# Kernel tuning notes

Measured on AMD Instinct MI355X. Metric: run time of the kernel, lower is better.

## Reference

```python
import jax, jax.numpy as jnp
import numpy as np

EPS = 1e-6
H, KV, HD = 16, 4, 64      # q heads, kv heads, head dim
BLK = 32                   # dllm_block_length (block-diffusion attention)
TOPK = 2                   # experts per token

def rmsnorm(x, w):
    return x * jax.lax.rsqrt(jnp.mean(x * x, axis=-1, keepdims=True) + EPS) * w

def rotate_half(x):
    x1, x2 = jnp.split(x, 2, axis=-1)
    return jnp.concatenate([-x2, x1], axis=-1)

def setup_inputs() -> dict:
    key = jax.random.key(0)
    ks = jax.random.split(key, 12)
    B, S, D = 1, 2048, 1024
    E, I = 8, 1024
    s = 0.02
    pos = jnp.arange(S, dtype=jnp.float32)
    inv_freq = 1.0 / (10000.0 ** (jnp.arange(0, HD, 2, dtype=jnp.float32) / HD))
    emb = jnp.concatenate([jnp.outer(pos, inv_freq)] * 2, axis=-1)  # [S, HD]
    return {
        'hidden_states': jax.random.normal(ks[0], (B, S, D), jnp.float32),
        'cos': jnp.cos(emb), 'sin': jnp.sin(emb),
        'w_qkv': jax.random.normal(ks[1], (D, (H + 2 * KV) * HD), jnp.float32) * s,
        'w_o': jax.random.normal(ks[2], (H * HD, D), jnp.float32) * s,
        'q_norm_w': jnp.ones((HD,), jnp.float32),
        'k_norm_w': jnp.ones((HD,), jnp.float32),
        'in_ln_w': jnp.ones((D,), jnp.float32),
        'post_ln_w': jnp.ones((D,), jnp.float32),
        'router_w': jax.random.normal(ks[3], (D, E), jnp.float32) * s,
        'w_gate': jax.random.normal(ks[4], (E, D, I), jnp.float32) * s,
        'w_up': jax.random.normal(ks[5], (E, D, I), jnp.float32) * s,
        'w_down': jax.random.normal(ks[6], (E, I, D), jnp.float32) * s,
        'ws_gate': jax.random.normal(ks[7], (D, I), jnp.float32) * s,
        'ws_up': jax.random.normal(ks[8], (D, I), jnp.float32) * s,
        'ws_down': jax.random.normal(ks[9], (I, D), jnp.float32) * s,
    }

def reference(hidden_states, cos, sin, w_qkv, w_o, q_norm_w, k_norm_w, in_ln_w,
              post_ln_w, router_w, w_gate, w_up, w_down, ws_gate, ws_up, ws_down):
    B, S, D = hidden_states.shape
    scale = HD ** -0.5
    # --- attention (pre-norm) ---
    h = rmsnorm(hidden_states, in_ln_w)
    qkv = h @ w_qkv
    q, k, v = jnp.split(qkv, [H * HD, (H + KV) * HD], axis=-1)
    q = q.reshape(B, S, H, HD); k = k.reshape(B, S, KV, HD); v = v.reshape(B, S, KV, HD)
    q = rmsnorm(q, q_norm_w); k = rmsnorm(k, k_norm_w)   # qk-norm per head
    c = cos[None, :, None, :]; sn = sin[None, :, None, :]
    q = q * c + rotate_half(q) * sn
    k = k * c + rotate_half(k) * sn
    rep = H // KV
    k = jnp.repeat(k, rep, axis=2); v = jnp.repeat(v, rep, axis=2)  # GQA expand
    scores = jnp.einsum('bqhd,bkhd->bhqk', q, k) * scale
    blk = jnp.arange(S) // BLK
    mask = blk[:, None] >= blk[None, :]   # block-causal: full attn inside block
    scores = jnp.where(mask[None, None], scores, jnp.float32(-1e30))
    p = jax.nn.softmax(scores, axis=-1)
    attn = jnp.einsum('bhqk,bkhd->bqhd', p, v).reshape(B, S, H * HD)
    x = hidden_states + attn @ w_o
    # --- MoE FFN (pre-norm) ---
    h2 = rmsnorm(x, post_ln_w)
    t = h2.reshape(B * S, D)
    logits = t.astype(jnp.float32) @ router_w.astype(jnp.float32)  # fp32 router
    probs = jax.nn.softmax(logits, axis=-1)
    topv, topi = jax.lax.top_k(probs, TOPK)
    topv = topv / jnp.sum(topv, axis=-1, keepdims=True)            # norm_topk_prob
    E = router_w.shape[1]
    w_tok = jnp.zeros((t.shape[0], E), jnp.float32).at[
        jnp.arange(t.shape[0])[:, None], topi].set(topv).astype(t.dtype)
    g = jnp.einsum('td,edi->tei', t, w_gate)
    u = jnp.einsum('td,edi->tei', t, w_up)
    eo = jnp.einsum('tei,eid->ted', jax.nn.silu(g) * u, w_down)
    moe = jnp.einsum('te,ted->td', w_tok, eo)
    shared = (jax.nn.silu(t @ ws_gate) * (t @ ws_up)) @ ws_down
    return x + (moe + shared).reshape(B, S, D)
```

## Files before the change

### kernel.cpp

```cpp
#include <hip/hip_runtime.h>
#include <hip/hip_bf16.h>
#include <math.h>

#define S 2048
#define D 1024
#define NH 16
#define NKV 4
#define HD 64
#define QKV_N 1536
#define NE 8
#define NI 1024
#define EPS 1e-6f

typedef __bf16 bf16_t;
typedef __bf16 __attribute__((may_alias)) abf16;
typedef __attribute__((ext_vector_type(8))) __bf16 bf16x8;
typedef __attribute__((ext_vector_type(4))) float f32x4;
union I4B8 { int4 i; bf16x8 v; bf16_t e[8]; };

__device__ __forceinline__ void gll16(const void* g, void* l) {
  __builtin_amdgcn_global_load_lds(
      (const __attribute__((address_space(1))) void*)g,
      (__attribute__((address_space(3))) void*)l, 16, 0, 0);
}


__global__ void rmsnorm_router_kernel(const float* __restrict__ in, const float* __restrict__ w,
                                      const float* __restrict__ rw,
                                      __hip_bfloat16* __restrict__ out16,
                                      int* __restrict__ topk_e, float* __restrict__ topk_w) {
  int t = blockIdx.x;
  int tid = threadIdx.x;
  const float* row = in + (size_t)t * D;
  float v[4];
  float ss = 0.f;
#pragma unroll
  for (int i = 0; i < 4; ++i) {
    v[i] = row[tid + i * 256];
    ss += v[i] * v[i];
  }
#pragma unroll
  for (int off = 32; off; off >>= 1) ss += __shfl_xor(ss, off);
  __shared__ float wsum[4];
  __shared__ float pl[4][NE];
  int wave = tid >> 6, lane = tid & 63;
  if (lane == 0) wsum[wave] = ss;
  __syncthreads();
  float tot = wsum[0] + wsum[1] + wsum[2] + wsum[3];
  float r = rsqrtf(tot / (float)D + EPS);
  float p[NE] = {};
#pragma unroll
  for (int i = 0; i < 4; ++i) {
    int d = tid + i * 256;
    float val = v[i] * r * w[d];
    out16[(size_t)t * D + d] = __float2bfloat16(val);
    const float* rwd = rw + (size_t)d * NE;
#pragma unroll
    for (int e = 0; e < NE; ++e) p[e] += val * rwd[e];
  }
#pragma unroll
  for (int off = 32; off; off >>= 1)
#pragma unroll
    for (int e = 0; e < NE; ++e) p[e] += __shfl_xor(p[e], off);
  if (lane == 0)
#pragma unroll
    for (int e = 0; e < NE; ++e) pl[wave][e] = p[e];
  __syncthreads();
  if (tid == 0) {
    float q[NE];
#pragma unroll
    for (int e = 0; e < NE; ++e) q[e] = pl[0][e] + pl[1][e] + pl[2][e] + pl[3][e];
    float mx = q[0];
#pragma unroll
    for (int e = 1; e < NE; ++e) mx = fmaxf(mx, q[e]);
    float ex[NE];
#pragma unroll
    for (int e = 0; e < NE; ++e) ex[e] = __expf(q[e] - mx);
    int e0 = 0;
#pragma unroll
    for (int e = 1; e < NE; ++e) if (ex[e] > ex[e0]) e0 = e;
    int e1 = (e0 == 0) ? 1 : 0;
#pragma unroll
    for (int e = 0; e < NE; ++e) if (e != e0 && ex[e] > ex[e1]) e1 = e;
    float w0 = ex[e0] / (ex[e0] + ex[e1]);
    float w1 = ex[e1] / (ex[e0] + ex[e1]);
    topk_e[2 * t] = e0;  topk_e[2 * t + 1] = e1;
    topk_w[2 * t] = w0;  topk_w[2 * t + 1] = w1;
  }
}

__global__ void transpose_all_kernel(
    const float* __restrict__ w_qkv, const float* __restrict__ w_o,
    const float* __restrict__ w_gate, const float* __restrict__ w_up,
    const float* __restrict__ w_down, const float* __restrict__ ws_gate,
    const float* __restrict__ ws_up, const float* __restrict__ ws_down,
    __hip_bfloat16* wqkvT, __hip_bfloat16* woT, __hip_bfloat16* wgT,
    __hip_bfloat16* wuT, __hip_bfloat16* wdT, __hip_bfloat16* wsgT,
    __hip_bfloat16* wsuT, __hip_bfloat16* wsdT,
    const float* __restrict__ hidden, const float* __restrict__ in_ln,
    __hip_bfloat16* __restrict__ hb_out) {
  int z = blockIdx.z;
  int tid = threadIdx.x;
  if (z == 29) {
    __shared__ float wsum[4];
    int base = ((int)blockIdx.y * 24 + (int)blockIdx.x) * 6;
    int wave = tid >> 6;
#pragma unroll
    for (int jj = 0; jj < 6; ++jj) {
      int t = base + jj;
      if (t < S) {
        const float* row = hidden + (size_t)t * D;
        float v[4];
        float ss = 0.f;
#pragma unroll
        for (int i = 0; i < 4; ++i) {
          v[i] = row[tid + i * 256];
          ss += v[i] * v[i];
        }
#pragma unroll
        for (int off = 32; off; off >>= 1) ss += __shfl_xor(ss, off);
        if ((tid & 63) == 0) wsum[wave] = ss;
        __syncthreads();
        float tot = wsum[0] + wsum[1] + wsum[2] + wsum[3];
        float r = rsqrtf(tot / (float)D + EPS);
#pragma unroll
        for (int i = 0; i < 4; ++i) {
          int d = tid + i * 256;
          hb_out[(size_t)t * D + d] = __float2bfloat16(v[i] * r * in_ln[d]);
        }
      }
      __syncthreads();
    }
    return;
  }
  __shared__ bf16_t tileb[64 * 66];
  const float* W; __hip_bfloat16* WT; int Kd, Nd;
  if (z == 0)       { W = w_qkv;  WT = wqkvT; Kd = D;  Nd = QKV_N; }
  else if (z == 1)  { W = w_o;    WT = woT;   Kd = D;  Nd = D; }
  else if (z < 10)  { int e = z - 2;  W = w_gate + (size_t)e * D * NI; WT = wgT + (size_t)e * D * NI; Kd = D;  Nd = NI; }
  else if (z < 18)  { int e = z - 10; W = w_up   + (size_t)e * D * NI; WT = wuT + (size_t)e * D * NI; Kd = D;  Nd = NI; }
  else if (z < 26)  { int e = z - 18; W = w_down + (size_t)e * NI * D; WT = wdT + (size_t)e * NI * D; Kd = NI; Nd = D; }
  else if (z == 26) { W = ws_gate; WT = wsgT; Kd = D;  Nd = NI; }
  else if (z == 27) { W = ws_up;   WT = wsuT; Kd = D;  Nd = NI; }
  else              { W = ws_down; WT = wsdT; Kd = NI; Nd = D; }
  int n0 = blockIdx.x * 64, k0 = blockIdx.y * 64;
  if (n0 >= Nd || k0 >= Kd) return;
  int nq = tid & 15;
  int kq = tid >> 4;
  bf16_t b[4][4];
#pragma unroll
  for (int i = 0; i < 4; ++i) {
    float4 v = *(const float4*)(W + (size_t)(k0 + kq * 4 + i) * Nd + n0 + nq * 4);
    b[i][0] = (bf16_t)v.x; b[i][1] = (bf16_t)v.y;
    b[i][2] = (bf16_t)v.z; b[i][3] = (bf16_t)v.w;
  }
#pragma unroll
  for (int j = 0; j < 4; ++j) {
    union { bf16_t e[2]; int q; } p0, p1;
    p0.e[0] = b[0][j]; p0.e[1] = b[1][j];
    p1.e[0] = b[2][j]; p1.e[1] = b[3][j];
    int nrow = nq * 4 + j;
    *(int*)&tileb[nrow * 66 + kq * 4]     = p0.q;
    *(int*)&tileb[nrow * 66 + kq * 4 + 2] = p1.q;
  }
  __syncthreads();
  int n = tid >> 2;
  int kc = (tid & 3) * 16;
  union { bf16_t e[16]; int4 q[2]; } pk;
#pragma unroll
  for (int r = 0; r < 8; ++r)
    *(int*)&pk.e[r * 2] = *(const int*)&tileb[n * 66 + kc + r * 2];
  int4* outp = (int4*)(WT + (size_t)(n0 + n) * Kd + k0 + kc);
  outp[0] = pk.q[0];
  outp[1] = pk.q[1];
}

__global__ __launch_bounds__(256) void mgemm_kernel(
    const __hip_bfloat16* __restrict__ A, const __hip_bfloat16* __restrict__ BT,
    const float* __restrict__ Cadd, float* __restrict__ C,
    int M, int N, int K,
    const int* __restrict__ counts, const int* __restrict__ offsets,
    const int* __restrict__ tok, int a_comp,
    const __hip_bfloat16* __restrict__ As2, const __hip_bfloat16* __restrict__ BTs2,
    float* __restrict__ Cs2) {
  __shared__ __align__(16) bf16_t Asd[2][128 * 32];
  __shared__ __align__(16) bf16_t Bsd[2][128 * 32];
  __shared__ int rowmap[128];
  int e = blockIdx.z;
  bool sh = (counts != nullptr) && (e == NE);
  int cnt = sh ? M : (counts ? counts[e] : M);
  int bm = blockIdx.y * 128;
  if (bm >= cnt) return;
  int bn = blockIdx.x * 128;
  int obase = sh ? 0 : (offsets ? offsets[e] : 0);
  const bf16_t* Ab = sh ? (const bf16_t*)As2 : (const bf16_t*)A;
  const bf16_t* BTe = sh ? (const bf16_t*)BTs2 : ((const bf16_t*)BT + (size_t)e * N * K);
  float* Cp = sh ? Cs2 : C;
  const int* toke = (!sh && tok) ? tok + e * S : nullptr;
  int acompe = sh ? 0 : a_comp;
  int tid = threadIdx.x;
  if (tid < 128) {
    int gp = bm + tid;
    int cp = gp < cnt ? gp : cnt - 1;
    rowmap[tid] = toke ? toke[cp] : (acompe ? obase + cp : cp);
  }
  __syncthreads();
  int wave = tid >> 6, lane = tid & 63;
  int quad = lane >> 4, l16 = lane & 15;
  int wm = wave >> 1, wn = wave & 1;
  int srow = tid >> 2, scol = (tid & 3) * 8;
  size_t aoff0 = (size_t)rowmap[srow] * K + scol;
  size_t aoff1 = (size_t)rowmap[64 + srow] * K + scol;
  size_t boff0 = (size_t)(bn + srow) * K + scol;
  size_t boff1 = (size_t)(bn + 64 + srow) * K + scol;
  f32x4 acc[4][4];
#pragma unroll
  for (int i = 0; i < 4; ++i)
#pragma unroll
    for (int j = 0; j < 4; ++j) acc[i][j] = (f32x4){0.f, 0.f, 0.f, 0.f};

  {
    char* AsB = (char*)Asd[0] + wave * 1024;
    char* BsB = (char*)Bsd[0] + wave * 1024;
    gll16(Ab + aoff0, AsB);
    gll16(Ab + aoff1, AsB + 4096);
    gll16(BTe + boff0, BsB);
    gll16(BTe + boff1, BsB + 4096);
  }
  for (int k0 = 0; k0 < K; k0 += 32) {
    int cur = (k0 >> 5) & 1;
    __syncthreads();
    if (k0 + 32 < K) {
      char* AsB = (char*)Asd[cur ^ 1] + wave * 1024;
      char* BsB = (char*)Bsd[cur ^ 1] + wave * 1024;
      gll16(Ab + aoff0 + k0 + 32, AsB);
      gll16(Ab + aoff1 + k0 + 32, AsB + 4096);
      gll16(BTe + boff0 + k0 + 32, BsB);
      gll16(BTe + boff1 + k0 + 32, BsB + 4096);
    }
    I4B8 af[4], bfr[4];
#pragma unroll
    for (int i = 0; i < 4; ++i)
      af[i].i = *(const int4*)(Asd[cur] + (wm * 64 + i * 16 + l16) * 32 + quad * 8);
#pragma unroll
    for (int j = 0; j < 4; ++j)
      bfr[j].i = *(const int4*)(Bsd[cur] + (wn * 64 + j * 16 + l16) * 32 + quad * 8);
#pragma unroll
    for (int i = 0; i < 4; ++i)
#pragma unroll
      for (int j = 0; j < 4; ++j)
        acc[i][j] = __builtin_amdgcn_mfma_f32_16x16x32_bf16(af[i].v, bfr[j].v, acc[i][j], 0, 0, 0);
  }
#pragma unroll
  for (int i = 0; i < 4; ++i) {
#pragma unroll
    for (int r = 0; r < 4; ++r) {
      int trow = wm * 64 + i * 16 + quad * 4 + r;
      int gp = bm + trow;
      if (gp < cnt) {
        size_t rowb = (size_t)(obase + gp) * N;
#pragma unroll
        for (int j = 0; j < 4; ++j) {
          int col = bn + wn * 64 + j * 16 + l16;
          size_t idx = rowb + col;
          Cp[idx] = acc[i][j][r] + (Cadd ? Cadd[idx] : 0.f);
        }
      }
    }
  }
}

__global__ __launch_bounds__(256) void mgemm_n64_kernel(
    const __hip_bfloat16* __restrict__ A, const __hip_bfloat16* __restrict__ BT,
    const float* __restrict__ Cadd, float* __restrict__ C,
    int M, int N, int K) {
  __shared__ __align__(16) bf16_t Asd[2][128 * 32];
  __shared__ __align__(16) bf16_t Bsd[2][64 * 32];
  int bm = blockIdx.y * 128;
  int bn = blockIdx.x * 64;
  int tid = threadIdx.x;
  int wave = tid >> 6, lane = tid & 63;
  int quad = lane >> 4, l16 = lane & 15;
  int wm = wave >> 1, wn = wave & 1;
  int srow = tid >> 2, scol = (tid & 3) * 8;
  size_t aoff0 = (size_t)(bm + srow) * K + scol;
  size_t aoff1 = (size_t)(bm + 64 + srow) * K + scol;
  size_t boff = (size_t)(bn + srow) * K + scol;
  const bf16_t* Ab = (const bf16_t*)A;
  const bf16_t* Bb = (const bf16_t*)BT;
  f32x4 acc[4][2];
#pragma unroll
  for (int i = 0; i < 4; ++i)
#pragma unroll
    for (int j = 0; j < 2; ++j) acc[i][j] = (f32x4){0.f, 0.f, 0.f, 0.f};
  {
    char* AsB = (char*)Asd[0] + wave * 1024;
    gll16(Ab + aoff0, AsB);
    gll16(Ab + aoff1, AsB + 4096);
    gll16(Bb + boff, (char*)Bsd[0] + wave * 1024);
  }
  for (int k0 = 0; k0 < K; k0 += 32) {
    int cur = (k0 >> 5) & 1;
    __syncthreads();
    if (k0 + 32 < K) {
      char* AsB = (char*)Asd[cur ^ 1] + wave * 1024;
      gll16(Ab + aoff0 + k0 + 32, AsB);
      gll16(Ab + aoff1 + k0 + 32, AsB + 4096);
      gll16(Bb + boff + k0 + 32, (char*)Bsd[cur ^ 1] + wave * 1024);
    }
    I4B8 af[4], bf[2];
#pragma unroll
    for (int i = 0; i < 4; ++i)
      af[i].i = *(const int4*)(Asd[cur] + (wm * 64 + i * 16 + l16) * 32 + quad * 8);
#pragma unroll
    for (int j = 0; j < 2; ++j)
      bf[j].i = *(const int4*)(Bsd[cur] + (wn * 32 + j * 16 + l16) * 32 + quad * 8);
#pragma unroll
    for (int i = 0; i < 4; ++i)
#pragma unroll
      for (int j = 0; j < 2; ++j)
        acc[i][j] = __builtin_amdgcn_mfma_f32_16x16x32_bf16(af[i].v, bf[j].v, acc[i][j], 0, 0, 0);
  }
#pragma unroll
  for (int i = 0; i < 4; ++i) {
#pragma unroll
    for (int r = 0; r < 4; ++r) {
      int gp = bm + wm * 64 + i * 16 + quad * 4 + r;
      size_t rowb = (size_t)gp * N;
#pragma unroll
      for (int j = 0; j < 2; ++j) {
        int col = bn + wn * 32 + j * 16 + l16;
        size_t idx = rowb + col;
        C[idx] = acc[i][j][r] + (Cadd ? Cadd[idx] : 0.f);
      }
    }
  }
}

__global__ __launch_bounds__(256) void mgemm_gu_kernel(
    const __hip_bfloat16* __restrict__ A, const __hip_bfloat16* __restrict__ BTg,
    const __hip_bfloat16* __restrict__ BTu, __hip_bfloat16* __restrict__ act,
    int M, int N, int K,
    const int* __restrict__ counts, const int* __restrict__ offsets,
    const int* __restrict__ tok,
    const __hip_bfloat16* __restrict__ BTgs, const __hip_bfloat16* __restrict__ BTus,
    __hip_bfloat16* __restrict__ acts) {
  __shared__ __align__(16) bf16_t Asd[2][128 * 32];
  __shared__ __align__(16) bf16_t Bgd[2][64 * 32];
  __shared__ __align__(16) bf16_t Bud[2][64 * 32];
  __shared__ int rowmap[128];
  int e = blockIdx.z;
  bool sh = (counts != nullptr) && (e == NE);
  int cnt = sh ? M : (counts ? counts[e] : M);
  int bm = blockIdx.y * 128;
  if (bm >= cnt) return;
  int bn = blockIdx.x * 64;
  const bf16_t* Ab = (const bf16_t*)A;
  const bf16_t* Bg = sh ? (const bf16_t*)BTgs : ((const bf16_t*)BTg + (size_t)e * N * K);
  const bf16_t* Bu = sh ? (const bf16_t*)BTus : ((const bf16_t*)BTu + (size_t)e * N * K);
  bf16_t* outp = sh ? (bf16_t*)acts : (bf16_t*)act;
  int obase = sh ? 0 : (offsets ? offsets[e] : 0);
  const int* toke = (!sh && tok) ? tok + e * S : nullptr;
  int tid = threadIdx.x;
  if (tid < 128) {
    int gp = bm + tid;
    int cp = gp < cnt ? gp : cnt - 1;
    rowmap[tid] = toke ? toke[cp] : cp;
  }
  __syncthreads();
  int wave = tid >> 6, lane = tid & 63;
  int quad = lane >> 4, l16 = lane & 15;
  int wm = wave >> 1, wn = wave & 1;
  int srow = tid >> 2, scol = (tid & 3) * 8;
  size_t aoff0 = (size_t)rowmap[srow] * K + scol;
  size_t aoff1 = (size_t)rowmap[64 + srow] * K + scol;
  size_t boff = (size_t)(bn + srow) * K + scol;
  f32x4 accg[4][2], accu[4][2];
#pragma unroll
  for (int i = 0; i < 4; ++i)
#pragma unroll
    for (int j = 0; j < 2; ++j) {
      accg[i][j] = (f32x4){0.f, 0.f, 0.f, 0.f};
      accu[i][j] = (f32x4){0.f, 0.f, 0.f, 0.f};
    }
  {
    char* AsB = (char*)Asd[0] + wave * 1024;
    gll16(Ab + aoff0, AsB);
    gll16(Ab + aoff1, AsB + 4096);
    gll16(Bg + boff, (char*)Bgd[0] + wave * 1024);
    gll16(Bu + boff, (char*)Bud[0] + wave * 1024);
  }
  for (int k0 = 0; k0 < K; k0 += 32) {
    int cur = (k0 >> 5) & 1;
    __syncthreads();
    if (k0 + 32 < K) {
      char* AsB = (char*)Asd[cur ^ 1] + wave * 1024;
      gll16(Ab + aoff0 + k0 + 32, AsB);
      gll16(Ab + aoff1 + k0 + 32, AsB + 4096);
      gll16(Bg + boff + k0 + 32, (char*)Bgd[cur ^ 1] + wave * 1024);
      gll16(Bu + boff + k0 + 32, (char*)Bud[cur ^ 1] + wave * 1024);
    }
    I4B8 af[4], bg[2], bu[2];
#pragma unroll
    for (int i = 0; i < 4; ++i)
      af[i].i = *(const int4*)(Asd[cur] + (wm * 64 + i * 16 + l16) * 32 + quad * 8);
#pragma unroll
    for (int j = 0; j < 2; ++j) {
      bg[j].i = *(const int4*)(Bgd[cur] + (wn * 32 + j * 16 + l16) * 32 + quad * 8);
      bu[j].i = *(const int4*)(Bud[cur] + (wn * 32 + j * 16 + l16) * 32 + quad * 8);
    }
#pragma unroll
    for (int i = 0; i < 4; ++i)
#pragma unroll
      for (int j = 0; j < 2; ++j) {
        accg[i][j] = __builtin_amdgcn_mfma_f32_16x16x32_bf16(af[i].v, bg[j].v, accg[i][j], 0, 0, 0);
        accu[i][j] = __builtin_amdgcn_mfma_f32_16x16x32_bf16(af[i].v, bu[j].v, accu[i][j], 0, 0, 0);
      }
  }
#pragma unroll
  for (int i = 0; i < 4; ++i) {
#pragma unroll
    for (int r = 0; r < 4; ++r) {
      int trow = wm * 64 + i * 16 + quad * 4 + r;
      int gp = bm + trow;
      if (gp < cnt) {
        size_t rowb = (size_t)(obase + gp) * N;
#pragma unroll
        for (int j = 0; j < 2; ++j) {
          int col = bn + wn * 32 + j * 16 + l16;
          float g = accg[i][j][r], uu = accu[i][j][r];
          float sg = g / (1.f + __expf(-g));
          outp[rowb + col] = __float2bfloat16(sg * uu);
        }
      }
    }
  }
}

__global__ void qkv_post_kernel(const float* __restrict__ qkv,
                                const float* __restrict__ qw, const float* __restrict__ kw,
                                const float* __restrict__ cosb, const float* __restrict__ sinb,
                                __hip_bfloat16* __restrict__ qout,
                                __hip_bfloat16* __restrict__ kout,
                                __hip_bfloat16* __restrict__ vT) {
  __shared__ float tile[32][33];
  if (blockIdx.y == 5) {
    int bx = blockIdx.x;
    if (bx < 512) {
      int t0 = (bx & 63) * 32;
      int c0 = (bx >> 6) * 32;
      int tx = threadIdx.x & 31, ty = threadIdx.x >> 5;
#pragma unroll
      for (int i = 0; i < 4; ++i)
        tile[ty + i * 8][tx] = qkv[(size_t)(t0 + ty + i * 8) * QKV_N + (NH + NKV) * HD + c0 + tx];
      __syncthreads();
#pragma unroll
      for (int i = 0; i < 4; ++i)
        vT[(size_t)(c0 + ty + i * 8) * S + t0 + tx] = __float2bfloat16(tile[tx][ty + i * 8]);
    }
    return;
  }
  int t = blockIdx.x;
  int u = blockIdx.y * 4 + (threadIdx.x >> 6);
  int lane = threadIdx.x & 63;
  bool isq = (u < NH);
  int h = isq ? u : (u - NH);
  size_t src = (size_t)t * QKV_N + (isq ? (h * HD) : (NH * HD + h * HD)) + lane;
  float xv = qkv[src];
  float ss = xv * xv;
#pragma unroll
  for (int off = 32; off; off >>= 1) ss += __shfl_xor(ss, off);
  float r = rsqrtf(ss * (1.f / 64.f) + EPS);
  float xn = xv * r * (isq ? qw[lane] : kw[lane]);
  float other = __shfl_xor(xn, 32);
  float rot = (lane < 32) ? -other : other;
  float res = xn * cosb[t * 64 + lane] + rot * sinb[t * 64 + lane];
  if (isq) qout[(size_t)t * (NH * HD) + h * HD + lane] = __float2bfloat16(res * 0.125f);
  else     kout[(size_t)t * (NKV * HD) + h * HD + lane] = __float2bfloat16(res);
}

__global__ __launch_bounds__(256) void attn_kernel(
    const __hip_bfloat16* __restrict__ qg, const __hip_bfloat16* __restrict__ kg,
    const __hip_bfloat16* __restrict__ vT,
    float* __restrict__ op0, float* __restrict__ op1,
    float* __restrict__ op2, float* __restrict__ op3,
    float* __restrict__ mpart, float* __restrict__ lpart) {
  int qt = (int)(gridDim.x - 1) - (int)blockIdx.x;
  int kvh = blockIdx.y;
  int z = blockIdx.z;
  int tid = threadIdx.x;
  int wave = tid >> 6, lane = tid & 63;
  int quad = lane >> 4, l16 = lane & 15;
  int h = kvh * 4 + wave;

  float* opz = (z == 0) ? op0 : (z == 1) ? op1 : (z == 2) ? op2 : op3;
  float* mp = mpart + (size_t)z * S * NH;
  float* lp = lpart + (size_t)z * S * NH;

  int nb = (qt >> 1) + 1;
  int nt = (nb + 1) >> 1;
  bool halfm = (nb & 1) != 0;
  int lo = (nt * z) >> 2;
  int hi = (nt * (z + 1)) >> 2;

  if (lo >= hi) {
    int row = qt * 16 + (tid >> 4);
    float* od = opz + (size_t)row * (NH * HD) + kvh * 256 + (tid & 15) * 16;
    int4 zz = {0, 0, 0, 0};
#pragma unroll
    for (int i = 0; i < 4; ++i) *(int4*)(od + i * 4) = zz;
    if (tid < 64) {
      int rr = qt * 16 + (tid >> 2), hh = kvh * 4 + (tid & 3);
      mp[(size_t)rr * NH + hh] = -1e30f;
      lp[(size_t)rr * NH + hh] = 0.f;
    }
    return;
  }

  __shared__ __align__(16) int KsI[64 * 36];
  __shared__ __align__(16) int VTI[64 * 36];
  __shared__ __align__(16) int PsI[4][16 * 36];

  I4B8 qf[2];
#pragma unroll
  for (int ch = 0; ch < 2; ++ch)
    qf[ch].i = *(const int4*)((const abf16*)qg +
        (size_t)(qt * 16 + l16) * (NH * HD) + h * HD + ch * 32 + quad * 8);

  I4B8 ones;
  ones.i = (int4){0x3F803F80, 0x3F803F80, 0x3F803F80, 0x3F803F80};

  float m_r[4];
  f32x4 o[4], o4;
#pragma unroll
  for (int r = 0; r < 4; ++r) m_r[r] = -1e30f;
#pragma unroll
  for (int sub = 0; sub < 4; ++sub) o[sub] = (f32x4){0.f, 0.f, 0.f, 0.f};
  o4 = (f32x4){0.f, 0.f, 0.f, 0.f};

  int sp = tid >> 3, sc = tid & 7;
  const abf16* kb = (const abf16*)kg;
  const abf16* vb = (const abf16*)vT;

  int4 rk0 = *(const int4*)(kb + (size_t)(lo * 64 + sp) * (NKV * HD) + kvh * HD + sc * 8);
  int4 rk1 = *(const int4*)(kb + (size_t)(lo * 64 + 32 + sp) * (NKV * HD) + kvh * HD + sc * 8);
  int4 rv0 = *(const int4*)(vb + (size_t)(kvh * HD + sp) * S + lo * 64 + sc * 8);
  int4 rv1 = *(const int4*)(vb + (size_t)(kvh * HD + 32 + sp) * S + lo * 64 + sc * 8);

  for (int kc = lo; kc < hi; ++kc) {
    *(int4*)&KsI[sp * 36 + sc * 4] = rk0;
    *(int4*)&KsI[(sp + 32) * 36 + sc * 4] = rk1;
    *(int4*)&VTI[sp * 36 + sc * 4] = rv0;
    *(int4*)&VTI[(sp + 32) * 36 + sc * 4] = rv1;
    __syncthreads();

    if (kc + 1 < hi) {
      rk0 = *(const int4*)(kb + (size_t)((kc + 1) * 64 + sp) * (NKV * HD) + kvh * HD + sc * 8);
      rk1 = *(const int4*)(kb + (size_t)((kc + 1) * 64 + 32 + sp) * (NKV * HD) + kvh * HD + sc * 8);
      rv0 = *(const int4*)(vb + (size_t)(kvh * HD + sp) * S + (kc + 1) * 64 + sc * 8);
      rv1 = *(const int4*)(vb + (size_t)(kvh * HD + 32 + sp) * S + (kc + 1) * 64 + sc * 8);
    }

    f32x4 s[4];
#pragma unroll
    for (int sub = 0; sub < 4; ++sub) s[sub] = (f32x4){0.f, 0.f, 0.f, 0.f};
    __builtin_amdgcn_s_setprio(1);
#pragma unroll
    for (int sub = 0; sub < 4; ++sub)
#pragma unroll
      for (int ch = 0; ch < 2; ++ch) {
        I4B8 ku;
        ku.i = *(const int4*)&KsI[(sub * 16 + l16) * 36 + ch * 16 + quad * 4];
        s[sub] = __builtin_amdgcn_mfma_f32_16x16x32_bf16(qf[ch].v, ku.v, s[sub], 0, 0, 0);
      }
    __builtin_amdgcn_s_setprio(0);
    if (halfm && kc == nt - 1) {
#pragma unroll
      for (int r = 0; r < 4; ++r) { s[2][r] = -1e30f; s[3][r] = -1e30f; }
    }

    abf16* pw = (abf16*)PsI[wave];
#pragma unroll
    for (int r = 0; r < 4; ++r) {
      float v = fmaxf(fmaxf(s[0][r], s[1][r]), fmaxf(s[2][r], s[3][r]));
#pragma unroll
      for (int off = 1; off < 16; off <<= 1) v = fmaxf(v, __shfl_xor(v, off));
      float mx = fmaxf(m_r[r], v);
      float al = __expf(m_r[r] - mx);
      m_r[r] = mx;
      float p0 = __expf(s[0][r] - mx);
      float p1 = __expf(s[1][r] - mx);
      float p2 = __expf(s[2][r] - mx);
      float p3 = __expf(s[3][r] - mx);
      int prow = quad * 4 + r;
      pw[prow * 72 + l16]      = (bf16_t)p0;
      pw[prow * 72 + 16 + l16] = (bf16_t)p1;
      pw[prow * 72 + 32 + l16] = (bf16_t)p2;
      pw[prow * 72 + 48 + l16] = (bf16_t)p3;
      o4[r] *= al;
#pragma unroll
      for (int sub = 0; sub < 4; ++sub) o[sub][r] *= al;
    }

    I4B8 pu[2];
#pragma unroll
    for (int ch = 0; ch < 2; ++ch)
      pu[ch].i = *(const int4*)&PsI[wave][l16 * 36 + ch * 16 + quad * 4];
    __builtin_amdgcn_s_setprio(1);
#pragma unroll
    for (int sub = 0; sub < 4; ++sub)
#pragma unroll
      for (int ch = 0; ch < 2; ++ch) {
        I4B8 vf;
        vf.i = *(const int4*)&VTI[(sub * 16 + l16) * 36 + ch * 16 + quad * 4];
        o[sub] = __builtin_amdgcn_mfma_f32_16x16x32_bf16(pu[ch].v, vf.v, o[sub], 0, 0, 0);
      }
#pragma unroll
    for (int ch = 0; ch < 2; ++ch)
      o4 = __builtin_amdgcn_mfma_f32_16x16x32_bf16(pu[ch].v, ones.v, o4, 0, 0, 0);
    __builtin_amdgcn_s_setprio(0);
    __syncthreads();
  }

#pragma unroll
  for (int r = 0; r < 4; ++r) {
    int row = qt * 16 + quad * 4 + r;
    float* od = opz + (size_t)row * (NH * HD) + h * HD;
#pragma unroll
    for (int sub = 0; sub < 4; ++sub)
      od[sub * 16 + l16] = o[sub][r];
    if (l16 == 0) {
      mp[(size_t)row * NH + h] = m_r[r];
      lp[(size_t)row * NH + h] = o4[r];
    }
  }
}

__global__ void attn_merge_kernel(const float* __restrict__ op0,
                                  const float* __restrict__ op1,
                                  const float* __restrict__ op2,
                                  const float* __restrict__ op3,
                                  const float* __restrict__ mpart,
                                  const float* __restrict__ lpart,
                                  __hip_bfloat16* __restrict__ attn) {
  int row = blockIdx.x;
  int tid = threadIdx.x;
#pragma unroll
  for (int i = 0; i < 4; ++i) {
    int c = tid + i * 256;
    int h = c >> 6;
    float m0 = mpart[(size_t)row * NH + h];
    float m1 = mpart[(size_t)(S + row) * NH + h];
    float m2 = mpart[(size_t)(2 * S + row) * NH + h];
    float m3 = mpart[(size_t)(3 * S + row) * NH + h];
    float l0 = lpart[(size_t)row * NH + h];
    float l1 = lpart[(size_t)(S + row) * NH + h];
    float l2 = lpart[(size_t)(2 * S + row) * NH + h];
    float l3 = lpart[(size_t)(3 * S + row) * NH + h];
    float M = fmaxf(fmaxf(m0, m1), fmaxf(m2, m3));
    float a0 = __expf(m0 - M), a1 = __expf(m1 - M);
    float a2 = __expf(m2 - M), a3 = __expf(m3 - M);
    float l = l0 * a0 + l1 * a1 + l2 * a2 + l3 * a3;
    size_t idx = (size_t)row * (NH * HD) + c;
    float v = (op0[idx] * a0 + op1[idx] * a1 + op2[idx] * a2 + op3[idx] * a3) / l;
    attn[idx] = __float2bfloat16(v);
  }
}

__global__ __launch_bounds__(1024) void router_place_kernel(
    const int* __restrict__ topk_e, int* __restrict__ counts, int* __restrict__ offsets,
    int* __restrict__ tok_list, int* __restrict__ topk_pos) {
  __shared__ int lcnt[NE];
  int tid = threadIdx.x;
  int lane = tid & 63;
  if (tid < NE) lcnt[tid] = 0;
  __syncthreads();
#pragma unroll
  for (int r = 0; r < 2; ++r) {
    int t = r * 1024 + tid;
#pragma unroll
    for (int s = 0; s < 2; ++s) {
      int e = topk_e[2 * t + s];
      int pos = 0;
#pragma unroll
      for (int x = 0; x < NE; ++x) {
        unsigned long long mask = __ballot(e == x);
        if (mask) {
          int leader = __ffsll((unsigned long long)mask) - 1;
          int cnt = __popcll(mask);
          int base = 0;
          if (lane == leader) base = atomicAdd(&lcnt[x], cnt);
          base = __shfl(base, leader);
          if (e == x)
            pos = base + __popcll(mask & ((1ull << lane) - 1ull));
        }
      }
      topk_pos[2 * t + s] = pos;
      tok_list[e * S + pos] = t;
    }
  }
  __syncthreads();
  if (tid == 0) {
    int acc = 0;
    for (int e = 0; e < NE; ++e) { offsets[e] = acc; counts[e] = lcnt[e]; acc += lcnt[e]; }
  }
}

__global__ void final_kernel(const float* __restrict__ x, const float* __restrict__ sout,
                             const float* __restrict__ eo,
                             const int* __restrict__ topk_e, const int* __restrict__ topk_pos,
                             const float* __restrict__ topk_w, const int* __restrict__ offsets,
                             float* __restrict__ out) {
  int t = blockIdx.x;
  int tid = threadIdx.x;
  int e0 = topk_e[2 * t], e1 = topk_e[2 * t + 1];
  size_t r0 = (size_t)offsets[e0] + topk_pos[2 * t];
  size_t r1 = (size_t)offsets[e1] + topk_pos[2 * t + 1];
  float w0 = topk_w[2 * t], w1 = topk_w[2 * t + 1];
#pragma unroll
  for (int i = 0; i < 4; ++i) {
    int d = tid + i * 256;
    size_t idx = (size_t)t * D + d;
    out[idx] = x[idx] + sout[idx] + w0 * eo[r0 * D + d] + w1 * eo[r1 * D + d];
  }
}

extern "C" void kernel_launch(void* const* d_in, const int* in_sizes, int n_in,
                              void* d_out, int out_size, void* d_ws, size_t ws_size,
                              hipStream_t stream) {
  const float* hidden  = (const float*)d_in[0];
  const float* cosb    = (const float*)d_in[1];
  const float* sinb    = (const float*)d_in[2];
  const float* w_qkv   = (const float*)d_in[3];
  const float* w_o     = (const float*)d_in[4];
  const float* q_norm  = (const float*)d_in[5];
  const float* k_norm  = (const float*)d_in[6];
  const float* in_ln   = (const float*)d_in[7];
  const float* post_ln = (const float*)d_in[8];
  const float* router_w= (const float*)d_in[9];
  const float* w_gate  = (const float*)d_in[10];
  const float* w_up    = (const float*)d_in[11];
  const float* w_down  = (const float*)d_in[12];
  const float* ws_gate = (const float*)d_in[13];
  const float* ws_up   = (const float*)d_in[14];
  const float* ws_down = (const float*)d_in[15];
  float* out = (float*)d_out;
  float* ws = (float*)d_ws;

  typedef __hip_bfloat16 hbf;
  hbf* wqkvT = (hbf*)(ws);
  hbf* woT   = (hbf*)(ws +  768 * 1024);
  hbf* wgT   = (hbf*)(ws + 1280 * 1024);
  hbf* wuT   = (hbf*)(ws + 5376 * 1024);
  hbf* wdT   = (hbf*)(ws + 9472 * 1024);
  hbf* wsgT  = (hbf*)(ws + 13568 * 1024);
  hbf* wsuT  = (hbf*)(ws + 14080 * 1024);
  hbf* wsdT  = (hbf*)(ws + 14592 * 1024);
  hbf*   hb      = (hbf*)(ws + 15104 * 1024);
  float* qkv     = ws + 16128 * 1024;
  hbf*   qbB     = (hbf*)(ws + 19200 * 1024);
  hbf*   kbB     = (hbf*)(ws + 20224 * 1024);
  hbf*   vTb     = (hbf*)(ws + 20480 * 1024);
  hbf*   attnb16 = (hbf*)(ws + 20736 * 1024);
  float* x       = ws + 22784 * 1024;
  hbf*   h2b     = (hbf*)(ws + 26880 * 1024);
  hbf*   act     = (hbf*)(ws + 16128 * 1024);
  float* eo      = ws + 18176 * 1024;
  hbf*   sact    = (hbf*)(ws + 27904 * 1024);
  float* sout    = ws + 28928 * 1024;
  float* mpart   = ws + 15104 * 1024;
  float* lpart   = mpart + 4 * S * NH;
  float* opart0  = ws + 16128 * 1024;
  float* opart1  = ws + 22784 * 1024;
  float* opart2  = ws + 28928 * 1024;
  float* opart3  = ws + 26880 * 1024;
  int* counts   = (int*)(ws + 30976 * 1024);
  int* offsets  = counts + NE;
  int* tok_list = offsets + NE;
  int* topk_e   = tok_list + NE * S;
  int* topk_pos = topk_e + 2 * S;
  float* topk_w = (float*)(topk_pos + 2 * S);

  dim3 b256(256);
  transpose_all_kernel<<<dim3(24, 16, 30), b256, 0, stream>>>(
      w_qkv, w_o, w_gate, w_up, w_down, ws_gate, ws_up, ws_down,
      wqkvT, woT, wgT, wuT, wdT, wsgT, wsuT, wsdT,
      hidden, in_ln, hb);
  mgemm_n64_kernel<<<dim3(QKV_N/64, S/128), b256, 0, stream>>>(hb, wqkvT, nullptr, qkv,
      S, QKV_N, D);
  qkv_post_kernel<<<dim3(S, 6), b256, 0, stream>>>(qkv, q_norm, k_norm, cosb, sinb, qbB, kbB, vTb);
  attn_kernel<<<dim3(S/16, NKV, 4), b256, 0, stream>>>(qbB, kbB, vTb,
      opart0, opart1, opart2, opart3, mpart, lpart);
  attn_merge_kernel<<<S, b256, 0, stream>>>(opart0, opart1, opart2, opart3,
      mpart, lpart, attnb16);
  mgemm_n64_kernel<<<dim3(D/64, S/128), b256, 0, stream>>>(attnb16, woT, hidden, x,
      S, D, D);
  rmsnorm_router_kernel<<<S, b256, 0, stream>>>(x, post_ln, router_w, h2b, topk_e, topk_w);
  router_place_kernel<<<1, 1024, 0, stream>>>(topk_e, counts, offsets, tok_list, topk_pos);
  mgemm_gu_kernel<<<dim3(NI/64, S/128, NE + 1), b256, 0, stream>>>(h2b, wgT, wuT, act,
      S, NI, D, counts, offsets, tok_list, wsgT, wsuT, sact);
  mgemm_kernel<<<dim3(D/128, S/128, NE + 1), b256, 0, stream>>>(act, wdT, nullptr, eo,
      S, D, NI, counts, offsets, nullptr, 1, sact, wsdT, sout);
  final_kernel<<<S, b256, 0, stream>>>(x, sout, eo, topk_e, topk_pos, topk_w, offsets, out);
}
```

Before: 394.9 us.

## Fuse split-KV attention merge into attention kernel via last-block atomic counter

Removes the separate attn_merge launch. Each attention block increments a per-query-tile atomic counter, and the last of the 16 blocks for that tile (4 kv heads × 4 splits) merges the partial outputs into the bf16 attention result. The counters are zeroed inside the transpose kernel. This saves a kernel launch and lets the merge overlap with other attention work. In exchange it adds fences and atomics, and the merge is serialized within one block per tile, which may run slowly at the tail.

```diff
diff --git a/kernel.cpp b/kernel.cpp
--- a/kernel.cpp
+++ b/kernel.cpp
@@ -98,10 +98,11 @@
     __hip_bfloat16* wuT, __hip_bfloat16* wdT, __hip_bfloat16* wsgT,
     __hip_bfloat16* wsuT, __hip_bfloat16* wsdT,
     const float* __restrict__ hidden, const float* __restrict__ in_ln,
-    __hip_bfloat16* __restrict__ hb_out) {
+    __hip_bfloat16* __restrict__ hb_out, int* __restrict__ qt_ctr) {
   int z = blockIdx.z;
   int tid = threadIdx.x;
   if (z == 29) {
+    if (blockIdx.x == 0 && blockIdx.y == 0 && tid < 128) qt_ctr[tid] = 0;
     __shared__ float wsum[4];
     int base = ((int)blockIdx.y * 24 + (int)blockIdx.x) * 6;
     int wave = tid >> 6;
@@ -484,7 +485,8 @@
     const __hip_bfloat16* __restrict__ vT,
     float* __restrict__ op0, float* __restrict__ op1,
     float* __restrict__ op2, float* __restrict__ op3,
-    float* __restrict__ mpart, float* __restrict__ lpart) {
+    float* __restrict__ mpart, float* __restrict__ lpart,
+    __hip_bfloat16* __restrict__ attn_out, int* __restrict__ qt_ctr) {
   int qt = (int)(gridDim.x - 1) - (int)blockIdx.x;
   int kvh = blockIdx.y;
   int z = blockIdx.z;
@@ -493,6 +495,11 @@
   int quad = lane >> 4, l16 = lane & 15;
   int h = kvh * 4 + wave;
 
+  __shared__ __align__(16) int KsI[64 * 36];
+  __shared__ __align__(16) int VTI[64 * 36];
+  __shared__ __align__(16) int PsI[4][16 * 36];
+  __shared__ int lastFlag;
+
   float* opz = (z == 0) ? op0 : (z == 1) ? op1 : (z == 2) ? op2 : op3;
   float* mp = mpart + (size_t)z * S * NH;
   float* lp = lpart + (size_t)z * S * NH;
@@ -514,156 +521,154 @@
       mp[(size_t)rr * NH + hh] = -1e30f;
       lp[(size_t)rr * NH + hh] = 0.f;
     }
-    return;
-  }
-
-  __shared__ __align__(16) int KsI[64 * 36];
-  __shared__ __align__(16) int VTI[64 * 36];
-  __shared__ __align__(16) int PsI[4][16 * 36];
-
-  I4B8 qf[2];
-#pragma unroll
-  for (int ch = 0; ch < 2; ++ch)
-    qf[ch].i = *(const int4*)((const abf16*)qg +
-        (size_t)(qt * 16 + l16) * (NH * HD) + h * HD + ch * 32 + quad * 8);
-
-  I4B8 ones;
-  ones.i = (int4){0x3F803F80, 0x3F803F80, 0x3F803F80, 0x3F803F80};
-
-  float m_r[4];
-  f32x4 o[4], o4;
-#pragma unroll
-  for (int r = 0; r < 4; ++r) m_r[r] = -1e30f;
-#pragma unroll
-  for (int sub = 0; sub < 4; ++sub) o[sub] = (f32x4){0.f, 0.f, 0.f, 0.f};
-  o4 = (f32x4){0.f, 0.f, 0.f, 0.f};
-
-  int sp = tid >> 3, sc = tid & 7;
-  const abf16* kb = (const abf16*)kg;
-  const abf16* vb = (const abf16*)vT;
-
-  int4 rk0 = *(const int4*)(kb + (size_t)(lo * 64 + sp) * (NKV * HD) + kvh * HD + sc * 8);
-  int4 rk1 = *(const int4*)(kb + (size_t)(lo * 64 + 32 + sp) * (NKV * HD) + kvh * HD + sc * 8);
-  int4 rv0 = *(const int4*)(vb + (size_t)(kvh * HD + sp) * S + lo * 64 + sc * 8);
-  int4 rv1 = *(const int4*)(vb + (size_t)(kvh * HD + 32 + sp) * S + lo * 64 + sc * 8);
-
-  for (int kc = lo; kc < hi; ++kc) {
-    *(int4*)&KsI[sp * 36 + sc * 4] = rk0;
-    *(int4*)&KsI[(sp + 32) * 36 + sc * 4] = rk1;
-    *(int4*)&VTI[sp * 36 + sc * 4] = rv0;
-    *(int4*)&VTI[(sp + 32) * 36 + sc * 4] = rv1;
-    __syncthreads();
-
-    if (kc + 1 < hi) {
-      rk0 = *(const int4*)(kb + (size_t)((kc + 1) * 64 + sp) * (NKV * HD) + kvh * HD + sc * 8);
-      rk1 = *(const int4*)(kb + (size_t)((kc + 1) * 64 + 32 + sp) * (NKV * HD) + kvh * HD + sc * 8);
-      rv0 = *(const int4*)(vb + (size_t)(kvh * HD + sp) * S + (kc + 1) * 64 + sc * 8);
-      rv1 = *(const int4*)(vb + (size_t)(kvh * HD + 32 + sp) * S + (kc + 1) * 64 + sc * 8);
-    }
-
-    f32x4 s[4];
-#pragma unroll
-    for (int sub = 0; sub < 4; ++sub) s[sub] = (f32x4){0.f, 0.f, 0.f, 0.f};
-    __builtin_amdgcn_s_setprio(1);
-#pragma unroll
-    for (int sub = 0; sub < 4; ++sub)
-#pragma unroll
-      for (int ch = 0; ch < 2; ++ch) {
-        I4B8 ku;
-        ku.i = *(const int4*)&KsI[(sub * 16 + l16) * 36 + ch * 16 + quad * 4];
-        s[sub] = __builtin_amdgcn_mfma_f32_16x16x32_bf16(qf[ch].v, ku.v, s[sub], 0, 0, 0);
-      }
-    __builtin_amdgcn_s_setprio(0);
-    if (halfm && kc == nt - 1) {
-#pragma unroll
-      for (int r = 0; r < 4; ++r) { s[2][r] = -1e30f; s[3][r] = -1e30f; }
-    }
-
-    abf16* pw = (abf16*)PsI[wave];
+  } else {
+    I4B8 qf[2];
+#pragma unroll
+    for (int ch = 0; ch < 2; ++ch)
+      qf[ch].i = *(const int4*)((const abf16*)qg +
+          (size_t)(qt * 16 + l16) * (NH * HD) + h * HD + ch * 32 + quad * 8);
+
+    I4B8 ones;
+    ones.i = (int4){0x3F803F80, 0x3F803F80, 0x3F803F80, 0x3F803F80};
+
+    float m_r[4];
+    f32x4 o[4], o4;
+#pragma unroll
+    for (int r = 0; r < 4; ++r) m_r[r] = -1e30f;
+#pragma unroll
+    for (int sub = 0; sub < 4; ++sub) o[sub] = (f32x4){0.f, 0.f, 0.f, 0.f};
+    o4 = (f32x4){0.f, 0.f, 0.f, 0.f};
+
+    int sp = tid >> 3, sc = tid & 7;
+    const abf16* kb = (const abf16*)kg;
+    const abf16* vb = (const abf16*)vT;
+
+    int4 rk0 = *(const int4*)(kb + (size_t)(lo * 64 + sp) * (NKV * HD) + kvh * HD + sc * 8);
+    int4 rk1 = *(const int4*)(kb + (size_t)(lo * 64 + 32 + sp) * (NKV * HD) + kvh * HD + sc * 8);
+    int4 rv0 = *(const int4*)(vb + (size_t)(kvh * HD + sp) * S + lo * 64 + sc * 8);
+    int4 rv1 = *(const int4*)(vb + (size_t)(kvh * HD + 32 + sp) * S + lo * 64 + sc * 8);
+
+    for (int kc = lo; kc < hi; ++kc) {
+      *(int4*)&KsI[sp * 36 + sc * 4] = rk0;
+      *(int4*)&KsI[(sp + 32) * 36 + sc * 4] = rk1;
+      *(int4*)&VTI[sp * 36 + sc * 4] = rv0;
+      *(int4*)&VTI[(sp + 32) * 36 + sc * 4] = rv1;
+      __syncthreads();
+
+      if (kc + 1 < hi) {
+        rk0 = *(const int4*)(kb + (size_t)((kc + 1) * 64 + sp) * (NKV * HD) + kvh * HD + sc * 8);
+        rk1 = *(const int4*)(kb + (size_t)((kc + 1) * 64 + 32 + sp) * (NKV * HD) + kvh * HD + sc * 8);
+        rv0 = *(const int4*)(vb + (size_t)(kvh * HD + sp) * S + (kc + 1) * 64 + sc * 8);
+        rv1 = *(const int4*)(vb + (size_t)(kvh * HD + 32 + sp) * S + (kc + 1) * 64 + sc * 8);
+      }
+
+      f32x4 s[4];
+#pragma unroll
+      for (int sub = 0; sub < 4; ++sub) s[sub] = (f32x4){0.f, 0.f, 0.f, 0.f};
+      __builtin_amdgcn_s_setprio(1);
+#pragma unroll
+      for (int sub = 0; sub < 4; ++sub)
+#pragma unroll
+        for (int ch = 0; ch < 2; ++ch) {
+          I4B8 ku;
+          ku.i = *(const int4*)&KsI[(sub * 16 + l16) * 36 + ch * 16 + quad * 4];
+          s[sub] = __builtin_amdgcn_mfma_f32_16x16x32_bf16(qf[ch].v, ku.v, s[sub], 0, 0, 0);
+        }
+      __builtin_amdgcn_s_setprio(0);
+      if (halfm && kc == nt - 1) {
+#pragma unroll
+        for (int r = 0; r < 4; ++r) { s[2][r] = -1e30f; s[3][r] = -1e30f; }
+      }
+
+      abf16* pw = (abf16*)PsI[wave];
+#pragma unroll
+      for (int r = 0; r < 4; ++r) {
+        float v = fmaxf(fmaxf(s[0][r], s[1][r]), fmaxf(s[2][r], s[3][r]));
+#pragma unroll
+        for (int off = 1; off < 16; off <<= 1) v = fmaxf(v, __shfl_xor(v, off));
+        float mx = fmaxf(m_r[r], v);
+        float al = __expf(m_r[r] - mx);
+        m_r[r] = mx;
+        float p0 = __expf(s[0][r] - mx);
+        float p1 = __expf(s[1][r] - mx);
+        float p2 = __expf(s[2][r] - mx);
+        float p3 = __expf(s[3][r] - mx);
+        int prow = quad * 4 + r;
+        pw[prow * 72 + l16]      = (bf16_t)p0;
+        pw[prow * 72 + 16 + l16] = (bf16_t)p1;
+        pw[prow * 72 + 32 + l16] = (bf16_t)p2;
+        pw[prow * 72 + 48 + l16] = (bf16_t)p3;
+        o4[r] *= al;
+#pragma unroll
+        for (int sub = 0; sub < 4; ++sub) o[sub][r] *= al;
+      }
+
+      I4B8 pu[2];
+#pragma unroll
+      for (int ch = 0; ch < 2; ++ch)
+        pu[ch].i = *(const int4*)&PsI[wave][l16 * 36 + ch * 16 + quad * 4];
+      __builtin_amdgcn_s_setprio(1);
+#pragma unroll
+      for (int sub = 0; sub < 4; ++sub)
+#pragma unroll
+        for (int ch = 0; ch < 2; ++ch) {
+          I4B8 vf;
+          vf.i = *(const int4*)&VTI[(sub * 16 + l16) * 36 + ch * 16 + quad * 4];
+          o[sub] = __builtin_amdgcn_mfma_f32_16x16x32_bf16(pu[ch].v, vf.v, o[sub], 0, 0, 0);
+        }
+#pragma unroll
+      for (int ch = 0; ch < 2; ++ch)
+        o4 = __builtin_amdgcn_mfma_f32_16x16x32_bf16(pu[ch].v, ones.v, o4, 0, 0, 0);
+      __builtin_amdgcn_s_setprio(0);
+      __syncthreads();
+    }
+
 #pragma unroll
     for (int r = 0; r < 4; ++r) {
-      float v = fmaxf(fmaxf(s[0][r], s[1][r]), fmaxf(s[2][r], s[3][r]));
-#pragma unroll
-      for (int off = 1; off < 16; off <<= 1) v = fmaxf(v, __shfl_xor(v, off));
-      float mx = fmaxf(m_r[r], v);
-      float al = __expf(m_r[r] - mx);
-      m_r[r] = mx;
-      float p0 = __expf(s[0][r] - mx);
-      float p1 = __expf(s[1][r] - mx);
-      float p2 = __expf(s[2][r] - mx);
-      float p3 = __expf(s[3][r] - mx);
-      int prow = quad * 4 + r;
-      pw[prow * 72 + l16]      = (bf16_t)p0;
-      pw[prow * 72 + 16 + l16] = (bf16_t)p1;
-      pw[prow * 72 + 32 + l16] = (bf16_t)p2;
-      pw[prow * 72 + 48 + l16] = (bf16_t)p3;
-      o4[r] *= al;
-#pragma unroll
-      for (int sub = 0; sub < 4; ++sub) o[sub][r] *= al;
-    }
-
-    I4B8 pu[2];
-#pragma unroll
-    for (int ch = 0; ch < 2; ++ch)
-      pu[ch].i = *(const int4*)&PsI[wave][l16 * 36 + ch * 16 + quad * 4];
-    __builtin_amdgcn_s_setprio(1);
-#pragma unroll
-    for (int sub = 0; sub < 4; ++sub)
-#pragma unroll
-      for (int ch = 0; ch < 2; ++ch) {
-        I4B8 vf;
-        vf.i = *(const int4*)&VTI[(sub * 16 + l16) * 36 + ch * 16 + quad * 4];
-        o[sub] = __builtin_amdgcn_mfma_f32_16x16x32_bf16(pu[ch].v, vf.v, o[sub], 0, 0, 0);
-      }
-#pragma unroll
-    for (int ch = 0; ch < 2; ++ch)
-      o4 = __builtin_amdgcn_mfma_f32_16x16x32_bf16(pu[ch].v, ones.v, o4, 0, 0, 0);
-    __builtin_amdgcn_s_setprio(0);
-    __syncthreads();
-  }
-
-#pragma unroll
-  for (int r = 0; r < 4; ++r) {
-    int row = qt * 16 + quad * 4 + r;
-    float* od = opz + (size_t)row * (NH * HD) + h * HD;
-#pragma unroll
-    for (int sub = 0; sub < 4; ++sub)
-      od[sub * 16 + l16] = o[sub][r];
-    if (l16 == 0) {
-      mp[(size_t)row * NH + h] = m_r[r];
-      lp[(size_t)row * NH + h] = o4[r];
-    }
-  }
-}
-
-__global__ void attn_merge_kernel(const float* __restrict__ op0,
-                                  const float* __restrict__ op1,
-                                  const float* __restrict__ op2,
-                                  const float* __restrict__ op3,
-                                  const float* __restrict__ mpart,
-                                  const float* __restrict__ lpart,
-                                  __hip_bfloat16* __restrict__ attn) {
-  int row = blockIdx.x;
-  int tid = threadIdx.x;
-#pragma unroll
-  for (int i = 0; i < 4; ++i) {
-    int c = tid + i * 256;
-    int h = c >> 6;
-    float m0 = mpart[(size_t)row * NH + h];
-    float m1 = mpart[(size_t)(S + row) * NH + h];
-    float m2 = mpart[(size_t)(2 * S + row) * NH + h];
-    float m3 = mpart[(size_t)(3 * S + row) * NH + h];
-    float l0 = lpart[(size_t)row * NH + h];
-    float l1 = lpart[(size_t)(S + row) * NH + h];
-    float l2 = lpart[(size_t)(2 * S + row) * NH + h];
-    float l3 = lpart[(size_t)(3 * S + row) * NH + h];
-    float M = fmaxf(fmaxf(m0, m1), fmaxf(m2, m3));
-    float a0 = __expf(m0 - M), a1 = __expf(m1 - M);
-    float a2 = __expf(m2 - M), a3 = __expf(m3 - M);
-    float l = l0 * a0 + l1 * a1 + l2 * a2 + l3 * a3;
-    size_t idx = (size_t)row * (NH * HD) + c;
-    float v = (op0[idx] * a0 + op1[idx] * a1 + op2[idx] * a2 + op3[idx] * a3) / l;
-    attn[idx] = __float2bfloat16(v);
+      int row = qt * 16 + quad * 4 + r;
+      float* od = opz + (size_t)row * (NH * HD) + h * HD;
+#pragma unroll
+      for (int sub = 0; sub < 4; ++sub)
+        od[sub * 16 + l16] = o[sub][r];
+      if (l16 == 0) {
+        mp[(size_t)row * NH + h] = m_r[r];
+        lp[(size_t)row * NH + h] = o4[r];
+      }
+    }
+  }
+
+  __syncthreads();
+  if (tid == 0) {
+    __threadfence();
+    int prev = atomicAdd(&qt_ctr[qt], 1);
+    lastFlag = (prev == NKV * 4 - 1);
+  }
+  __syncthreads();
+  if (lastFlag) {
+    __threadfence();
+    for (int rr = 0; rr < 16; ++rr) {
+      int row = qt * 16 + rr;
+#pragma unroll
+      for (int i = 0; i < 4; ++i) {
+        int c = tid + i * 256;
+        int hh = c >> 6;
+        float m0 = mpart[(size_t)row * NH + hh];
+        float m1 = mpart[(size_t)(S + row) * NH + hh];
+        float m2 = mpart[(size_t)(2 * S + row) * NH + hh];
+        float m3 = mpart[(size_t)(3 * S + row) * NH + hh];
+        float l0 = lpart[(size_t)row * NH + hh];
+        float l1 = lpart[(size_t)(S + row) * NH + hh];
+        float l2 = lpart[(size_t)(2 * S + row) * NH + hh];
+        float l3 = lpart[(size_t)(3 * S + row) * NH + hh];
+        float M = fmaxf(fmaxf(m0, m1), fmaxf(m2, m3));
+        float a0 = __expf(m0 - M), a1 = __expf(m1 - M);
+        float a2 = __expf(m2 - M), a3 = __expf(m3 - M);
+        float l = l0 * a0 + l1 * a1 + l2 * a2 + l3 * a3;
+        size_t idx = (size_t)row * (NH * HD) + c;
+        float v = (op0[idx] * a0 + op1[idx] * a1 + op2[idx] * a2 + op3[idx] * a3) / l;
+        attn_out[idx] = __float2bfloat16(v);
+      }
+    }
   }
 }
 
@@ -780,19 +785,18 @@
   int* topk_e   = tok_list + NE * S;
   int* topk_pos = topk_e + 2 * S;
   float* topk_w = (float*)(topk_pos + 2 * S);
+  int* qt_ctr   = (int*)(topk_w + 2 * S);
 
   dim3 b256(256);
   transpose_all_kernel<<<dim3(24, 16, 30), b256, 0, stream>>>(
       w_qkv, w_o, w_gate, w_up, w_down, ws_gate, ws_up, ws_down,
       wqkvT, woT, wgT, wuT, wdT, wsgT, wsuT, wsdT,
-      hidden, in_ln, hb);
+      hidden, in_ln, hb, qt_ctr);
   mgemm_n64_kernel<<<dim3(QKV_N/64, S/128), b256, 0, stream>>>(hb, wqkvT, nullptr, qkv,
       S, QKV_N, D);
   qkv_post_kernel<<<dim3(S, 6), b256, 0, stream>>>(qkv, q_norm, k_norm, cosb, sinb, qbB, kbB, vTb);
   attn_kernel<<<dim3(S/16, NKV, 4), b256, 0, stream>>>(qbB, kbB, vTb,
-      opart0, opart1, opart2, opart3, mpart, lpart);
-  attn_merge_kernel<<<S, b256, 0, stream>>>(opart0, opart1, opart2, opart3,
-      mpart, lpart, attnb16);
+      opart0, opart1, opart2, opart3, mpart, lpart, attnb16, qt_ctr);
   mgemm_n64_kernel<<<dim3(D/64, S/128), b256, 0, stream>>>(attnb16, woT, hidden, x,
       S, D, D);
   rmsnorm_router_kernel<<<S, b256, 0, stream>>>(x, post_ln, router_w, h2b, topk_e, topk_w);
```

New measurement: 496.1 us. +25.6%, slower.
